# Kernel optimization log

Hardware: AMD Instinct MI355X
Metric: run time of the kernel (lower is better)

The kernel has to match this reference:

```python
import jax, jax.numpy as jnp
import numpy as np

D_MODEL = 1024
N_HEADS = 16
D_K = D_MODEL // N_HEADS
D_FF = 4096
EPS = 1e-5


def setup_inputs() -> dict:
    key = jax.random.key(0)
    ks = jax.random.split(key, 16)
    s = 0.02
    d, f = D_MODEL, D_FF
    return {
        'ebd_x': jax.random.normal(ks[0], (2, 2048, d), jnp.float32),
        'Wq': jax.random.normal(ks[1], (d, d), jnp.float32) * s,
        'bq': jnp.zeros((d,), jnp.float32),
        'Wk': jax.random.normal(ks[2], (d, d), jnp.float32) * s,
        'bk': jnp.zeros((d,), jnp.float32),
        'Wv': jax.random.normal(ks[3], (d, d), jnp.float32) * s,
        'bv': jnp.zeros((d,), jnp.float32),
        'Wo': jax.random.normal(ks[4], (d, d), jnp.float32) * s,
        'bo': jnp.zeros((d,), jnp.float32),
        'W1': jax.random.normal(ks[5], (d, f), jnp.float32) * s,
        'b1': jnp.zeros((f,), jnp.float32),
        'W2': jax.random.normal(ks[6], (f, d), jnp.float32) * s,
        'b2': jnp.zeros((d,), jnp.float32),
        'g1': jnp.ones((d,), jnp.float32),
        'beta1': jnp.zeros((d,), jnp.float32),
        'g2': jnp.ones((d,), jnp.float32),
        'beta2': jnp.zeros((d,), jnp.float32),
    }


def _layernorm(x, g, b):
    mu = jnp.mean(x, axis=-1, keepdims=True)
    var = jnp.mean(jnp.square(x - mu), axis=-1, keepdims=True)
    return (x - mu) * jax.lax.rsqrt(var + EPS) * g + b


def reference(ebd_x, Wq, bq, Wk, bk, Wv, bv, Wo, bo, W1, b1, W2, b2, g1, beta1, g2, beta2):
    b, L, d = ebd_x.shape
    h, dk = N_HEADS, D_K
    # QKV projections, split heads: (b, h, L, dk)
    q = (ebd_x @ Wq + bq).reshape(b, L, h, dk).transpose(0, 2, 1, 3)
    k = (ebd_x @ Wk + bk).reshape(b, L, h, dk).transpose(0, 2, 1, 3)
    v = (ebd_x @ Wv + bv).reshape(b, L, h, dk).transpose(0, 2, 1, 3)
    scores = jnp.einsum('bhLd,bhld->bhLl', q, k) / jnp.sqrt(jnp.float32(dk))
    attn = jax.nn.softmax(scores, axis=-1)
    attn_v = jnp.einsum('bhLl,bhld->bhLd', attn, v)
    # faithful to source: reshape (b,h,L,dk) -> (b,L,d) WITHOUT transposing back
    attn_v = attn_v.reshape(b, L, d)
    attn_v = attn_v @ Wo + bo
    # dropout is identity in eval mode
    x1 = _layernorm(attn_v + ebd_x, g1, beta1)
    ff = jax.nn.gelu(x1 @ W1 + b1, approximate=False) @ W2 + b2
    return _layernorm(ff + x1, g2, beta2)
```

## Files before the change

### kernel.cpp

```cpp
#include <hip/hip_runtime.h>
#include <hip/hip_bf16.h>
#include <math.h>

typedef __bf16 bhalf;
typedef __bf16 bhalf8 __attribute__((ext_vector_type(8)));
typedef float  floatx4 __attribute__((ext_vector_type(4)));
typedef float  floatx8 __attribute__((ext_vector_type(8)));
typedef unsigned short ushort_t;
typedef unsigned short ushort8 __attribute__((ext_vector_type(8)));

#define MFMA16(a, b, c) __builtin_amdgcn_mfma_f32_16x16x32_bf16((a), (b), (c), 0, 0, 0)

__device__ __forceinline__ void gload_lds16(const bhalf* g, bhalf* l)
{
    __builtin_amdgcn_global_load_lds((const __attribute__((address_space(1))) void*)g,
                                     (__attribute__((address_space(3))) void*)l, 16, 0, 0);
}

enum { EPI_PLAIN = 0, EPI_RES = 1, EPI_GELU = 2, EPI_QKV = 3 };

__global__ __launch_bounds__(256) void detect_dtype(const ushort_t* __restrict__ x,
                                                    int* __restrict__ flag)
{
    __shared__ int tot;
    if (threadIdx.x == 0) tot = 0;
    __syncthreads();
    int cnt = 0;
#pragma unroll
    for (int it = 0; it < 8; ++it) {
        const ushort8 u = *(const ushort8*)(x + ((size_t)(it * 256 + threadIdx.x)) * 8);
#pragma unroll
        for (int j = 0; j < 8; j += 2) {
            const int e = (u[j] >> 7) & 0xFF;
            if (e >= 0x90) ++cnt;
        }
    }
    atomicAdd(&tot, cnt);
    __syncthreads();
    if (threadIdx.x == 0) flag[0] = (tot > 64) ? 1 : 0;
}

__global__ __launch_bounds__(256) void norm_x(const void* __restrict__ s,
                                              bhalf* __restrict__ d,
                                              const int* __restrict__ flag)
{
    const int i = (blockIdx.x * 256 + threadIdx.x) * 8;
    if (*flag) {
        const floatx8 v = *(const floatx8*)((const float*)s + i);
        bhalf8 o;
#pragma unroll
        for (int j = 0; j < 8; ++j) o[j] = (bhalf)v[j];
        *(bhalf8*)(d + i) = o;
    } else {
        *(ushort8*)((ushort_t*)d + i) = *(const ushort8*)((const ushort_t*)s + i);
    }
}

struct Cvt { const void* s; bhalf* d; int n; };
struct CvtArr { Cvt t[10]; };

__global__ __launch_bounds__(256) void norm_vec(CvtArr a, const int* __restrict__ flag)
{
    const Cvt c = a.t[blockIdx.y];
    const int i = (blockIdx.x * 256 + threadIdx.x) * 8;
    if (i >= c.n) return;
    if (*flag) {
        const floatx8 v = *(const floatx8*)((const float*)c.s + i);
        bhalf8 o;
#pragma unroll
        for (int j = 0; j < 8; ++j) o[j] = (bhalf)v[j];
        *(bhalf8*)(c.d + i) = o;
    } else {
        *(ushort8*)((ushort_t*)c.d + i) = *(const ushort8*)((const ushort_t*)c.s + i);
    }
}

struct TDesc { const void* src; bhalf* dst; int R, C; };
struct TDescArr { TDesc t[6]; };

__global__ __launch_bounds__(256) void transpose_all(TDescArr a, const int* __restrict__ flag)
{
    __shared__ bhalf sm[32][33];
    const int id = blockIdx.x;
    TDesc d;
    int rem;
    if (id < 4096)      { d = a.t[id >> 10]; rem = id & 1023; }
    else if (id < 8192) { d = a.t[4];        rem = id - 4096; }
    else                { d = a.t[5];        rem = id - 8192; }
    const int txc = d.C >> 5;
    const int bx = (rem % txc) * 32;
    const int by = (rem / txc) * 32;
    const int tx = threadIdx.x & 31;
    const int ty = threadIdx.x >> 5;
    if (*flag) {
        const float* fin = (const float*)d.src;
#pragma unroll
        for (int i = 0; i < 4; ++i)
            sm[ty + i * 8][tx] = (bhalf)fin[(size_t)(by + ty + i * 8) * d.C + bx + tx];
    } else {
        const bhalf* bin = (const bhalf*)d.src;
#pragma unroll
        for (int i = 0; i < 4; ++i)
            sm[ty + i * 8][tx] = bin[(size_t)(by + ty + i * 8) * d.C + bx + tx];
    }
    __syncthreads();
#pragma unroll
    for (int i = 0; i < 4; ++i)
        d.dst[(size_t)(bx + ty + i * 8) * d.R + by + tx] = sm[tx][ty + i * 8];
}

__global__ __launch_bounds__(256) void vt_transpose(const bhalf* __restrict__ Vw,
                                                    bhalf* __restrict__ Vt)
{
    __shared__ bhalf sm[32][33];
    const int bh = blockIdx.z;
    const int b = bh >> 4, h = bh & 15;
    const int tb = blockIdx.y * 32;
    const int db = blockIdx.x * 32;
    const int tx = threadIdx.x & 31;
    const int ty = threadIdx.x >> 5;
#pragma unroll
    for (int i = 0; i < 4; ++i)
        sm[ty + i * 8][tx] = Vw[(size_t)(b * 2048 + tb + ty + i * 8) * 1024 + h * 64 + db + tx];
    __syncthreads();
#pragma unroll
    for (int i = 0; i < 4; ++i)
        Vt[(size_t)(bh * 64 + db + ty + i * 8) * 2048 + tb + tx] = sm[tx][ty + i * 8];
}

template <int EPI, int TN>
__global__ __launch_bounds__(256) void gemm128(
    const bhalf* __restrict__ A, int lda,
    const bhalf* __restrict__ BT, int ldb,
    const bhalf* __restrict__ bias,
    const bhalf* __restrict__ resid,
    bhalf* __restrict__ C, int ldc, int K, int nbx,
    bhalf* __restrict__ Ck, bhalf* __restrict__ Cv)
{
    constexpr int MT = (TN == 128) ? 4 : 2;
    __shared__ __align__(16) bhalf As[2][128 * 64];
    __shared__ __align__(16) bhalf Bs[2][TN * 64];

    const int tid  = threadIdx.x;
    const int lane = tid & 63;
    const int w    = tid >> 6;
    const int l15  = lane & 15;
    const int q    = lane >> 4;
    const int wm   = (TN == 128) ? (w >> 1) * 64 : w * 32;
    const int wn   = (TN == 128) ? (w & 1) * 64 : 0;

    const int nwg = gridDim.x;
    const int cpx = nwg >> 3;
    const int id  = (blockIdx.x & 7) * cpx + (blockIdx.x >> 3);
    const int n0  = (id % nbx) * TN;
    const int m0  = (id / nbx) * 128;

    const int r8 = lane >> 3;
    const int c8 = lane & 7;
    const int gc = (c8 ^ r8) << 3;

    floatx4 acc[MT][4];
#pragma unroll
    for (int i = 0; i < MT; ++i)
#pragma unroll
        for (int j = 0; j < 4; ++j) acc[i][j] = (floatx4){0.f, 0.f, 0.f, 0.f};

    const bhalf* Ab = A  + (size_t)(m0 + r8) * lda + gc;
    const bhalf* Bb = BT + (size_t)(n0 + r8) * ldb + gc;

    auto stage = [&](int buf, int k0) {
#pragma unroll
        for (int i = 0; i < 4; ++i) {
            const int rb = w * 32 + i * 8;
            gload_lds16(Ab + (size_t)rb * lda + k0, &As[buf][rb * 64] + lane * 8);
        }
        if constexpr (TN == 128) {
#pragma unroll
            for (int i = 0; i < 4; ++i) {
                const int rb = w * 32 + i * 8;
                gload_lds16(Bb + (size_t)rb * ldb + k0, &Bs[buf][rb * 64] + lane * 8);
            }
        } else {
#pragma unroll
            for (int i = 0; i < 2; ++i) {
                const int rb = w * 16 + i * 8;
                gload_lds16(Bb + (size_t)rb * ldb + k0, &Bs[buf][rb * 64] + lane * 8);
            }
        }
    };

    auto compute = [&](int buf) {
#pragma unroll
        for (int s = 0; s < 2; ++s) {
            const int pc = (((s * 4 + q) ^ (l15 & 7)) << 3);
            bhalf8 af[MT], bf[4];
#pragma unroll
            for (int mt = 0; mt < MT; ++mt)
                af[mt] = *(const bhalf8*)&As[buf][(wm + mt * 16 + l15) * 64 + pc];
#pragma unroll
            for (int nt = 0; nt < 4; ++nt)
                bf[nt] = *(const bhalf8*)&Bs[buf][(wn + nt * 16 + l15) * 64 + pc];
#pragma unroll
            for (int mt = 0; mt < MT; ++mt)
#pragma unroll
                for (int nt = 0; nt < 4; ++nt)
                    acc[mt][nt] = MFMA16(af[mt], bf[nt], acc[mt][nt]);
        }
    };

    stage(0, 0);
    const int NT = K >> 6;
    for (int t = 0; t < NT; ++t) {
        const int cur = t & 1;
        if (t + 1 < NT) {
            stage(cur ^ 1, (t + 1) << 6);
            if constexpr (TN == 128)
                asm volatile("s_waitcnt vmcnt(8)" ::: "memory");
            else
                asm volatile("s_waitcnt vmcnt(6)" ::: "memory");
        } else {
            asm volatile("s_waitcnt vmcnt(0)" ::: "memory");
        }
        __builtin_amdgcn_s_barrier();
        asm volatile("" ::: "memory");
        compute(cur);
        if (t + 1 < NT) {
            asm volatile("" ::: "memory");
            __builtin_amdgcn_s_barrier();
            asm volatile("" ::: "memory");
        }
    }

#pragma unroll
    for (int mt = 0; mt < MT; ++mt)
#pragma unroll
        for (int nt = 0; nt < 4; ++nt) {
            const int col = n0 + wn + nt * 16 + l15;
            const float bv = (float)bias[col];
#pragma unroll
            for (int r = 0; r < 4; ++r) {
                const int row = m0 + wm + mt * 16 + q * 4 + r;
                float v = acc[mt][nt][r] + bv;
                if constexpr (EPI == EPI_RES) {
                    v += (float)resid[(size_t)row * ldc + col];
                    C[(size_t)row * ldc + col] = (bhalf)v;
                } else if constexpr (EPI == EPI_GELU) {
                    v = 0.5f * v * (1.f + erff(v * 0.70710678118654752f));
                    C[(size_t)row * ldc + col] = (bhalf)v;
                } else if constexpr (EPI == EPI_QKV) {
                    if (col < 1024)       C [(size_t)row * 1024 + col]        = (bhalf)v;
                    else if (col < 2048)  Ck[(size_t)row * 1024 + col - 1024] = (bhalf)v;
                    else                  Cv[(size_t)row * 1024 + col - 2048] = (bhalf)v;
                } else {
                    C[(size_t)row * ldc + col] = (bhalf)v;
                }
            }
        }
}

__global__ __launch_bounds__(256) void flash_attn(
    const bhalf* __restrict__ Q, const bhalf* __restrict__ Km,
    const bhalf* __restrict__ Vt, bhalf* __restrict__ ctx)
{
    __shared__ __align__(16) bhalf Ks[2][64 * 64];
    __shared__ __align__(16) bhalf Vs[2][64 * 64];

    const int tid  = threadIdx.x;
    const int lane = tid & 63;
    const int wq   = tid >> 6;
    const int l15  = lane & 15;
    const int q    = lane >> 4;
    const int bh   = blockIdx.x & 31;
    const int l0   = (blockIdx.x >> 5) * 64;
    const int b    = bh >> 4, h = bh & 15;
    const float SC = 0.125f * 1.44269504f;

    const bhalf* qp = Q + ((size_t)(b * 2048 + l0 + wq * 16 + l15)) * 1024 + h * 64 + q * 8;
    const bhalf8 aQ0 = *(const bhalf8*)qp;
    const bhalf8 aQ1 = *(const bhalf8*)(qp + 32);

    float ps = 0.f;
    floatx4 o[4];
#pragma unroll
    for (int ot = 0; ot < 4; ++ot) o[ot] = (floatx4){0.f, 0.f, 0.f, 0.f};

    const int r8 = lane >> 3;
    const int c8 = lane & 7;
    const bhalf* kbase = Km + ((size_t)(b * 2048)) * 1024 + h * 64;
    const bhalf* vbase = Vt + ((size_t)(bh * 64)) * 2048;

    auto stage = [&](int buf, int kt) {
#pragma unroll
        for (int i = 0; i < 2; ++i) {
            const int rb = wq * 16 + i * 8;
            const int fk = (((rb >> 3) << 1) ^ r8) & 7;
            gload_lds16(kbase + (size_t)(kt + rb + r8) * 1024 + ((c8 ^ fk) << 3),
                        &Ks[buf][rb * 64] + lane * 8);
            gload_lds16(vbase + (size_t)(rb + r8) * 2048 + kt + ((c8 ^ r8) << 3),
                        &Vs[buf][rb * 64] + lane * 8);
        }
    };

    stage(0, 0);
    int cur = 0;
    for (int kt = 0; kt < 2048; kt += 64) {
        __syncthreads();
        if (kt + 64 < 2048) stage(cur ^ 1, kt + 64);

        floatx4 s[4];
#pragma unroll
        for (int nt = 0; nt < 4; ++nt) {
            const int row = (nt >> 1) * 32 + (nt & 1) * 4 + ((l15 >> 2) << 3) + (l15 & 3);
            const int f = (((row >> 3) << 1) ^ row) & 7;
            const bhalf8 k0 = *(const bhalf8*)&Ks[cur][row * 64 + ((q ^ f) << 3)];
            const bhalf8 k1 = *(const bhalf8*)&Ks[cur][row * 64 + (((4 + q) ^ f) << 3)];
            floatx4 z = (floatx4){0.f, 0.f, 0.f, 0.f};
            z = MFMA16(k0, aQ0, z);
            s[nt] = MFMA16(k1, aQ1, z);
        }

        bhalf8 pa[2];
#pragma unroll
        for (int nt = 0; nt < 4; ++nt)
#pragma unroll
            for (int r = 0; r < 4; ++r) {
                const float pv = __builtin_amdgcn_exp2f(fmaf(s[nt][r], SC, -8.f));
                ps += pv;
                pa[nt >> 1][(nt & 1) * 4 + r] = (bhalf)pv;
            }

#pragma unroll
        for (int kc = 0; kc < 2; ++kc)
#pragma unroll
            for (int ot = 0; ot < 4; ++ot) {
                const bhalf8 bV = *(const bhalf8*)&Vs[cur][(ot * 16 + l15) * 64 + (((kc * 4 + q) ^ (l15 & 7)) << 3)];
                o[ot] = MFMA16(pa[kc], bV, o[ot]);
            }
        cur ^= 1;
    }

    ps += __shfl_xor(ps, 16);
    ps += __shfl_xor(ps, 32);
    const float invq = 1.f / ps;
    float inv[4];
#pragma unroll
    for (int r = 0; r < 4; ++r)
        inv[r] = __shfl(invq, (lane & 48) | (q * 4 + r));

#pragma unroll
    for (int ot = 0; ot < 4; ++ot)
#pragma unroll
        for (int r = 0; r < 4; ++r) {
            const int l = l0 + wq * 16 + q * 4 + r;
            const int kk = ot * 16 + l15;
            const int R = h * 128 + (l >> 4);
            const int Cc = (l & 15) * 64 + kk;
            ctx[((size_t)(b * 2048 + R)) * 1024 + Cc] = (bhalf)(o[ot][r] * inv[r]);
        }
}

__global__ __launch_bounds__(256) void ln_kernel(
    const bhalf* __restrict__ X, const bhalf* __restrict__ g,
    const bhalf* __restrict__ be, void* __restrict__ out, const int* __restrict__ flag)
{
    __shared__ float red[4][2];
    const int tid = threadIdx.x;
    const int wid = tid >> 6;
    const int rid = tid >> 7;
    const int lt  = tid & 127;
    const int row = blockIdx.x * 2 + rid;
    const int col = lt * 8;
    const bhalf8 xv = *(const bhalf8*)(X + (size_t)row * 1024 + col);
    float v[8], s1 = 0.f, s2 = 0.f;
#pragma unroll
    for (int i = 0; i < 8; ++i) {
        v[i] = (float)xv[i];
        s1 += v[i];
        s2 += v[i] * v[i];
    }
#pragma unroll
    for (int off = 1; off < 64; off <<= 1) {
        s1 += __shfl_xor(s1, off);
        s2 += __shfl_xor(s2, off);
    }
    if ((tid & 63) == 0) { red[wid][0] = s1; red[wid][1] = s2; }
    __syncthreads();
    const float t1 = red[rid * 2][0] + red[rid * 2 + 1][0];
    const float t2 = red[rid * 2][1] + red[rid * 2 + 1][1];
    const float mu = t1 * (1.f / 1024.f);
    const float rs = rsqrtf(t2 * (1.f / 1024.f) - mu * mu + 1e-5f);
    const bool f32 = flag && (*flag != 0);
    if (f32) {
        floatx8 ov;
#pragma unroll
        for (int i = 0; i < 8; ++i)
            ov[i] = ((v[i] - mu) * rs) * (float)g[col + i] + (float)be[col + i];
        *(floatx8*)((float*)out + (size_t)row * 1024 + col) = ov;
    } else {
        bhalf8 ov;
#pragma unroll
        for (int i = 0; i < 8; ++i)
            ov[i] = (bhalf)(((v[i] - mu) * rs) * (float)g[col + i] + (float)be[col + i]);
        *(bhalf8*)((bhalf*)out + (size_t)row * 1024 + col) = ov;
    }
}

extern "C" void kernel_launch(void* const* d_in, const int* in_sizes, int n_in,
                              void* d_out, int out_size, void* d_ws, size_t ws_size,
                              hipStream_t stream)
{
    (void)in_sizes; (void)n_in; (void)out_size; (void)ws_size;

    char* p = (char*)d_ws;
    const size_t MB = 1024 * 1024;
    int*   flag  = (int*)p;
    bhalf* vecs  = (bhalf*)(p + 128 * 1024);
    bhalf* Qw    = (bhalf*)(p + 1 * MB);
    bhalf* Kw    = (bhalf*)(p + 9 * MB);
    bhalf* Vw    = (bhalf*)(p + 17 * MB);
    bhalf* Vt    = (bhalf*)(p + 25 * MB);
    bhalf* x_n   = (bhalf*)(p + 33 * MB);
    bhalf* WqkvT = (bhalf*)(p + 41 * MB);
    bhalf* WoT   = (bhalf*)(p + 47 * MB);
    bhalf* W1T   = (bhalf*)(p + 49 * MB);
    bhalf* W2T   = (bhalf*)(p + 57 * MB);
    bhalf* ctx   = Vw;
    bhalf* ff1   = (bhalf*)(p + 17 * MB);
    bhalf* ln1   = Qw;
    bhalf* x1    = Kw;
    bhalf* ff2   = Qw;

    bhalf* bqkv  = vecs;
    bhalf* bo_n  = vecs + 1 * 4096;
    bhalf* b1_n  = vecs + 2 * 4096;
    bhalf* b2_n  = vecs + 3 * 4096;
    bhalf* g1_n  = vecs + 4 * 4096;
    bhalf* be1_n = vecs + 5 * 4096;
    bhalf* g2_n  = vecs + 6 * 4096;
    bhalf* be2_n = vecs + 7 * 4096;

    const dim3 blk(256);

    detect_dtype<<<1, blk, 0, stream>>>((const ushort_t*)d_in[0], flag);

    norm_x<<<2048, blk, 0, stream>>>(d_in[0], x_n, flag);
    CvtArr arr;
    arr.t[0] = {d_in[2],  bqkv,        1024};
    arr.t[1] = {d_in[4],  bqkv + 1024, 1024};
    arr.t[2] = {d_in[6],  bqkv + 2048, 1024};
    arr.t[3] = {d_in[8],  bo_n,        1024};
    arr.t[4] = {d_in[10], b1_n,        4096};
    arr.t[5] = {d_in[12], b2_n,        1024};
    arr.t[6] = {d_in[13], g1_n,        1024};
    arr.t[7] = {d_in[14], be1_n,       1024};
    arr.t[8] = {d_in[15], g2_n,        1024};
    arr.t[9] = {d_in[16], be2_n,       1024};
    norm_vec<<<dim3(2, 10), blk, 0, stream>>>(arr, flag);

    TDescArr td;
    td.t[0] = {d_in[1],  WqkvT,               1024, 1024};
    td.t[1] = {d_in[3],  WqkvT + 1024 * 1024, 1024, 1024};
    td.t[2] = {d_in[5],  WqkvT + 2048 * 1024, 1024, 1024};
    td.t[3] = {d_in[7],  WoT,                 1024, 1024};
    td.t[4] = {d_in[9],  W1T,                 1024, 4096};
    td.t[5] = {d_in[11], W2T,                 4096, 1024};
    transpose_all<<<12288, blk, 0, stream>>>(td, flag);

    gemm128<EPI_QKV, 128><<<768, blk, 0, stream>>>(
        x_n, 1024, WqkvT, 1024, bqkv, nullptr, Qw, 1024, 1024, 24, Kw, Vw);

    vt_transpose<<<dim3(2, 64, 32), blk, 0, stream>>>(Vw, Vt);

    flash_attn<<<1024, blk, 0, stream>>>(Qw, Kw, Vt, ctx);

    gemm128<EPI_RES, 64><<<512, blk, 0, stream>>>(
        ctx, 1024, WoT, 1024, bo_n, x_n, ln1, 1024, 1024, 16, nullptr, nullptr);
    ln_kernel<<<2048, blk, 0, stream>>>(ln1, g1_n, be1_n, x1, nullptr);

    gemm128<EPI_GELU, 128><<<1024, blk, 0, stream>>>(
        x1, 1024, W1T, 1024, b1_n, nullptr, ff1, 4096, 1024, 32, nullptr, nullptr);
    gemm128<EPI_RES, 64><<<512, blk, 0, stream>>>(
        ff1, 4096, W2T, 4096, b2_n, x1, ff2, 1024, 4096, 16, nullptr, nullptr);
    ln_kernel<<<2048, blk, 0, stream>>>(ff2, g2_n, be2_n, d_out, flag);
}
```

Baseline: 377.5 us.

## Restructure GEMM into 4-stage K=32 pipeline with precomputed swizzled offsets

The double-buffered K=64 GEMM main loop becomes a four-buffer ring with K=32 slices. Loads run three stages ahead, and the vmcnt waits are tuned per tile shape. LDS and global addresses are precomputed once with a new 4-way XOR swizzle, and the MFMA block is wrapped in s_setprio to favour issue. The aim is to hide global-load latency better, at the cost of twice as many barriers per unit of K and smaller MFMA bursts between syncs.

Result: slower. 414.9 us (+9.9%).

```diff
diff --git a/kernel.cpp b/kernel.cpp
--- a/kernel.cpp
+++ b/kernel.cpp
@@ -129,7 +129,7 @@
 }
 
 template <int EPI, int TN>
-__global__ __launch_bounds__(256) void gemm128(
+__global__ __launch_bounds__(256) void gemm_p4(
     const bhalf* __restrict__ A, int lda,
     const bhalf* __restrict__ BT, int ldb,
     const bhalf* __restrict__ bias,
@@ -137,9 +137,12 @@
     bhalf* __restrict__ C, int ldc, int K, int nbx,
     bhalf* __restrict__ Ck, bhalf* __restrict__ Cv)
 {
-    constexpr int MT = (TN == 128) ? 4 : 2;
-    __shared__ __align__(16) bhalf As[2][128 * 64];
-    __shared__ __align__(16) bhalf Bs[2][TN * 64];
+    constexpr int MT     = (TN == 128) ? 4 : 2;
+    constexpr int BLOADS = (TN == 128) ? 2 : 1;
+    constexpr int WS     = (TN == 128) ? 8 : 6;
+    constexpr int WT     = (TN == 128) ? 4 : 3;
+    __shared__ __align__(16) bhalf As[4][128 * 32];
+    __shared__ __align__(16) bhalf Bs[4][TN * 32];
 
     const int tid  = threadIdx.x;
     const int lane = tid & 63;
@@ -155,9 +158,33 @@
     const int n0  = (id % nbx) * TN;
     const int m0  = (id / nbx) * 128;
 
-    const int r8 = lane >> 3;
-    const int c8 = lane & 7;
-    const int gc = (c8 ^ r8) << 3;
+    const int sr = lane >> 2;
+    const int sl = lane & 3;
+
+    const bhalf* ga[2]; int la[2];
+#pragma unroll
+    for (int i = 0; i < 2; ++i) {
+        const int r = i * 64 + w * 16 + sr;
+        const int c = sl ^ (r & 3) ^ ((r >> 2) & 3);
+        ga[i] = A + (size_t)(m0 + r) * lda + c * 8;
+        la[i] = r * 32 + sl * 8;
+    }
+    const bhalf* gb[BLOADS]; int lb[BLOADS];
+#pragma unroll
+    for (int i = 0; i < BLOADS; ++i) {
+        const int r = (TN == 128) ? (i * 64 + w * 16 + sr) : (w * 16 + sr);
+        const int c = sl ^ (r & 3) ^ ((r >> 2) & 3);
+        gb[i] = BT + (size_t)(n0 + r) * ldb + c * 8;
+        lb[i] = r * 32 + sl * 8;
+    }
+
+    int oa[MT], ob[4];
+#pragma unroll
+    for (int mt = 0; mt < MT; ++mt)
+        oa[mt] = (wm + mt * 16 + l15) * 32 + ((q ^ (l15 & 3) ^ ((l15 >> 2) & 3)) * 8);
+#pragma unroll
+    for (int nt = 0; nt < 4; ++nt)
+        ob[nt] = (wn + nt * 16 + l15) * 32 + ((q ^ (l15 & 3) ^ ((l15 >> 2) & 3)) * 8);
 
     floatx4 acc[MT][4];
 #pragma unroll
@@ -165,70 +192,49 @@
 #pragma unroll
         for (int j = 0; j < 4; ++j) acc[i][j] = (floatx4){0.f, 0.f, 0.f, 0.f};
 
-    const bhalf* Ab = A  + (size_t)(m0 + r8) * lda + gc;
-    const bhalf* Bb = BT + (size_t)(n0 + r8) * ldb + gc;
-
-    auto stage = [&](int buf, int k0) {
-#pragma unroll
-        for (int i = 0; i < 4; ++i) {
-            const int rb = w * 32 + i * 8;
-            gload_lds16(Ab + (size_t)rb * lda + k0, &As[buf][rb * 64] + lane * 8);
-        }
-        if constexpr (TN == 128) {
-#pragma unroll
-            for (int i = 0; i < 4; ++i) {
-                const int rb = w * 32 + i * 8;
-                gload_lds16(Bb + (size_t)rb * ldb + k0, &Bs[buf][rb * 64] + lane * 8);
-            }
-        } else {
-#pragma unroll
-            for (int i = 0; i < 2; ++i) {
-                const int rb = w * 16 + i * 8;
-                gload_lds16(Bb + (size_t)rb * ldb + k0, &Bs[buf][rb * 64] + lane * 8);
-            }
-        }
+    auto stage = [&](int buf, int kt) {
+#pragma unroll
+        for (int i = 0; i < 2; ++i)
+            gload_lds16(ga[i] + kt, &As[buf][la[i]]);
+#pragma unroll
+        for (int i = 0; i < BLOADS; ++i)
+            gload_lds16(gb[i] + kt, &Bs[buf][lb[i]]);
     };
 
     auto compute = [&](int buf) {
-#pragma unroll
-        for (int s = 0; s < 2; ++s) {
-            const int pc = (((s * 4 + q) ^ (l15 & 7)) << 3);
-            bhalf8 af[MT], bf[4];
-#pragma unroll
-            for (int mt = 0; mt < MT; ++mt)
-                af[mt] = *(const bhalf8*)&As[buf][(wm + mt * 16 + l15) * 64 + pc];
+        bhalf8 af[MT], bf[4];
+#pragma unroll
+        for (int mt = 0; mt < MT; ++mt) af[mt] = *(const bhalf8*)&As[buf][oa[mt]];
+#pragma unroll
+        for (int nt = 0; nt < 4; ++nt) bf[nt] = *(const bhalf8*)&Bs[buf][ob[nt]];
+        __builtin_amdgcn_s_setprio(1);
+#pragma unroll
+        for (int mt = 0; mt < MT; ++mt)
 #pragma unroll
             for (int nt = 0; nt < 4; ++nt)
-                bf[nt] = *(const bhalf8*)&Bs[buf][(wn + nt * 16 + l15) * 64 + pc];
-#pragma unroll
-            for (int mt = 0; mt < MT; ++mt)
-#pragma unroll
-                for (int nt = 0; nt < 4; ++nt)
-                    acc[mt][nt] = MFMA16(af[mt], bf[nt], acc[mt][nt]);
-        }
+                acc[mt][nt] = MFMA16(af[mt], bf[nt], acc[mt][nt]);
+        __builtin_amdgcn_s_setprio(0);
     };
 
     stage(0, 0);
-    const int NT = K >> 6;
+    stage(1, 32);
+    stage(2, 64);
+    const int NT = K >> 5;
     for (int t = 0; t < NT; ++t) {
-        const int cur = t & 1;
-        if (t + 1 < NT) {
-            stage(cur ^ 1, (t + 1) << 6);
-            if constexpr (TN == 128)
-                asm volatile("s_waitcnt vmcnt(8)" ::: "memory");
-            else
-                asm volatile("s_waitcnt vmcnt(6)" ::: "memory");
-        } else {
+        if (t + 3 < NT) {
+            stage((t + 3) & 3, (t + 3) << 5);
+            asm volatile("s_waitcnt vmcnt(%0)" :: "i"(WS) : "memory");
+        } else if (t + 3 == NT) {
+            asm volatile("s_waitcnt vmcnt(%0)" :: "i"(WT) : "memory");
+        } else if (t + 2 == NT) {
             asm volatile("s_waitcnt vmcnt(0)" ::: "memory");
         }
         __builtin_amdgcn_s_barrier();
         asm volatile("" ::: "memory");
-        compute(cur);
-        if (t + 1 < NT) {
-            asm volatile("" ::: "memory");
-            __builtin_amdgcn_s_barrier();
-            asm volatile("" ::: "memory");
-        }
+        compute(t & 3);
+        asm volatile("" ::: "memory");
+        __builtin_amdgcn_s_barrier();
+        asm volatile("" ::: "memory");
     }
 
 #pragma unroll
@@ -466,20 +472,20 @@
     td.t[5] = {d_in[11], W2T,                 4096, 1024};
     transpose_all<<<12288, blk, 0, stream>>>(td, flag);
 
-    gemm128<EPI_QKV, 128><<<768, blk, 0, stream>>>(
+    gemm_p4<EPI_QKV, 128><<<768, blk, 0, stream>>>(
         x_n, 1024, WqkvT, 1024, bqkv, nullptr, Qw, 1024, 1024, 24, Kw, Vw);
 
     vt_transpose<<<dim3(2, 64, 32), blk, 0, stream>>>(Vw, Vt);
 
     flash_attn<<<1024, blk, 0, stream>>>(Qw, Kw, Vt, ctx);
 
-    gemm128<EPI_RES, 64><<<512, blk, 0, stream>>>(
+    gemm_p4<EPI_RES, 64><<<512, blk, 0, stream>>>(
         ctx, 1024, WoT, 1024, bo_n, x_n, ln1, 1024, 1024, 16, nullptr, nullptr);
     ln_kernel<<<2048, blk, 0, stream>>>(ln1, g1_n, be1_n, x1, nullptr);
 
-    gemm128<EPI_GELU, 128><<<1024, blk, 0, stream>>>(
+    gemm_p4<EPI_GELU, 128><<<1024, blk, 0, stream>>>(
         x1, 1024, W1T, 1024, b1_n, nullptr, ff1, 4096, 1024, 32, nullptr, nullptr);
-    gemm128<EPI_RES, 64><<<512, blk, 0, stream>>>(
+    gemm_p4<EPI_RES, 64><<<512, blk, 0, stream>>>(
         ff1, 4096, W2T, 4096, b2_n, x1, ff2, 1024, 4096, 16, nullptr, nullptr);
     ln_kernel<<<2048, blk, 0, stream>>>(ff2, g2_n, be2_n, d_out, flag);
 }
```

## Add 512-thread triple-buffered 128x128 GEMM for the W2 down-projection

Applied to the files above, without the earlier changes.

Adds a new gemm_pp kernel with 8 waves per 512-thread block, 128x128 output tiles, a three-stage LDS ring buffer fed by direct global-to-LDS loads with a two-tile prefetch distance, and raised wave priority around the MFMA section. It replaces the 128x64-tile gemm128 launch for the K=4096 FF2 projection, halving the block count to 256 and raising per-block reuse. The aim is to hide global-load latency and improve arithmetic intensity on this long-K GEMM. In exchange it needs 96KB of dynamic LDS (set once through a static attribute call) and leaves only one block per CU on 256 CUs, which may reduce latency hiding.

Result: faster. 369.6 us (-2.1%).

```diff
diff --git a/kernel.cpp b/kernel.cpp
--- a/kernel.cpp
+++ b/kernel.cpp
@@ -235,6 +235,133 @@
     for (int mt = 0; mt < MT; ++mt)
 #pragma unroll
         for (int nt = 0; nt < 4; ++nt) {
+            const int col = n0 + wn + nt * 16 + l15;
+            const float bv = (float)bias[col];
+#pragma unroll
+            for (int r = 0; r < 4; ++r) {
+                const int row = m0 + wm + mt * 16 + q * 4 + r;
+                float v = acc[mt][nt][r] + bv;
+                if constexpr (EPI == EPI_RES) {
+                    v += (float)resid[(size_t)row * ldc + col];
+                    C[(size_t)row * ldc + col] = (bhalf)v;
+                } else if constexpr (EPI == EPI_GELU) {
+                    v = 0.5f * v * (1.f + erff(v * 0.70710678118654752f));
+                    C[(size_t)row * ldc + col] = (bhalf)v;
+                } else if constexpr (EPI == EPI_QKV) {
+                    if (col < 1024)       C [(size_t)row * 1024 + col]        = (bhalf)v;
+                    else if (col < 2048)  Ck[(size_t)row * 1024 + col - 1024] = (bhalf)v;
+                    else                  Cv[(size_t)row * 1024 + col - 2048] = (bhalf)v;
+                } else {
+                    C[(size_t)row * ldc + col] = (bhalf)v;
+                }
+            }
+        }
+}
+
+template <int EPI>
+__global__ __launch_bounds__(512, 2) void gemm_pp(
+    const bhalf* __restrict__ A, int lda,
+    const bhalf* __restrict__ BT, int ldb,
+    const bhalf* __restrict__ bias,
+    const bhalf* __restrict__ resid,
+    bhalf* __restrict__ C, int ldc, int K, int nbx,
+    bhalf* __restrict__ Ck, bhalf* __restrict__ Cv)
+{
+    extern __shared__ __align__(16) bhalf sm[];
+
+    const int tid  = threadIdx.x;
+    const int lane = tid & 63;
+    const int w    = tid >> 6;
+    const int l15  = lane & 15;
+    const int q    = lane >> 4;
+    const int wm   = (w >> 2) * 64;
+    const int wn   = (w & 3) * 32;
+
+    const int nwg = gridDim.x;
+    const int cpx = nwg >> 3;
+    const int id  = (blockIdx.x & 7) * cpx + (blockIdx.x >> 3);
+    const int n0  = (id % nbx) * 128;
+    const int m0  = (id / nbx) * 128;
+
+    const int r6  = tid >> 3;
+    const int c8t = tid & 7;
+    const bhalf* gA[2]; const bhalf* gB[2]; int lA[2], lB[2];
+#pragma unroll
+    for (int i = 0; i < 2; ++i) {
+        const int row = i * 64 + r6;
+        const int gc  = (c8t ^ (r6 & 7)) << 3;
+        gA[i] = A  + (size_t)(m0 + row) * lda + gc;
+        gB[i] = BT + (size_t)(n0 + row) * ldb + gc;
+        lA[i] = row * 64 + c8t * 8;
+        lB[i] = row * 64 + c8t * 8;
+    }
+
+    floatx4 acc[4][2];
+#pragma unroll
+    for (int i = 0; i < 4; ++i)
+#pragma unroll
+        for (int j = 0; j < 2; ++j) acc[i][j] = (floatx4){0.f, 0.f, 0.f, 0.f};
+
+    auto stage = [&](int buf, int k0) {
+        bhalf* as = sm + buf * 8192;
+        bhalf* bs = sm + 24576 + buf * 8192;
+        gload_lds16(gA[0] + k0, as + lA[0]);
+        gload_lds16(gA[1] + k0, as + lA[1]);
+        gload_lds16(gB[0] + k0, bs + lB[0]);
+        gload_lds16(gB[1] + k0, bs + lB[1]);
+    };
+
+    stage(0, 0);
+    stage(1, 64);
+    asm volatile("s_waitcnt vmcnt(4)" ::: "memory");
+    __builtin_amdgcn_s_barrier();
+    asm volatile("" ::: "memory");
+
+    const int NT = K >> 6;
+    for (int t = 0; t < NT; ++t) {
+        const int buf = t % 3;
+        const bhalf* as = sm + buf * 8192;
+        const bhalf* bs = sm + 24576 + buf * 8192;
+
+        bhalf8 af[2][4], bf[2][2];
+#pragma unroll
+        for (int ks = 0; ks < 2; ++ks) {
+            const int pc = (((ks * 4 + q) ^ (l15 & 7)) << 3);
+#pragma unroll
+            for (int mt = 0; mt < 4; ++mt)
+                af[ks][mt] = *(const bhalf8*)&as[(wm + mt * 16 + l15) * 64 + pc];
+#pragma unroll
+            for (int nt = 0; nt < 2; ++nt)
+                bf[ks][nt] = *(const bhalf8*)&bs[(wn + nt * 16 + l15) * 64 + pc];
+        }
+
+        if (t + 2 < NT) stage((t + 2) % 3, (t + 2) << 6);
+
+        __builtin_amdgcn_s_setprio(1);
+#pragma unroll
+        for (int ks = 0; ks < 2; ++ks)
+#pragma unroll
+            for (int mt = 0; mt < 4; ++mt)
+#pragma unroll
+                for (int nt = 0; nt < 2; ++nt)
+                    acc[mt][nt] = MFMA16(af[ks][mt], bf[ks][nt], acc[mt][nt]);
+        __builtin_amdgcn_s_setprio(0);
+
+        if (t + 2 < NT) {
+            asm volatile("s_waitcnt vmcnt(4)" ::: "memory");
+        } else if (t + 1 < NT) {
+            asm volatile("s_waitcnt vmcnt(0)" ::: "memory");
+        }
+        if (t + 1 < NT) {
+            __builtin_amdgcn_s_barrier();
+            asm volatile("" ::: "memory");
+        }
+    }
+
+#pragma unroll
+    for (int mt = 0; mt < 4; ++mt)
+#pragma unroll
+        for (int nt = 0; nt < 2; ++nt) {
             const int col = n0 + wn + nt * 16 + l15;
             const float bv = (float)bias[col];
 #pragma unroll
@@ -439,7 +566,15 @@
     bhalf* g2_n  = vecs + 6 * 4096;
     bhalf* be2_n = vecs + 7 * 4096;
 
+    static bool attr_done = false;
+    if (!attr_done) {
+        hipFuncSetAttribute((const void*)gemm_pp<EPI_RES>,
+                            hipFuncAttributeMaxDynamicSharedMemorySize, 98304);
+        attr_done = true;
+    }
+
     const dim3 blk(256);
+    const dim3 blk512(512);
 
     detect_dtype<<<1, blk, 0, stream>>>((const ushort_t*)d_in[0], flag);
 
@@ -479,7 +614,7 @@
 
     gemm128<EPI_GELU, 128><<<1024, blk, 0, stream>>>(
         x1, 1024, W1T, 1024, b1_n, nullptr, ff1, 4096, 1024, 32, nullptr, nullptr);
-    gemm128<EPI_RES, 64><<<512, blk, 0, stream>>>(
-        ff1, 4096, W2T, 4096, b2_n, x1, ff2, 1024, 4096, 16, nullptr, nullptr);
+    gemm_pp<EPI_RES><<<256, blk512, 98304, stream>>>(
+        ff1, 4096, W2T, 4096, b2_n, x1, ff2, 1024, 4096, 8, nullptr, nullptr);
     ln_kernel<<<2048, blk, 0, stream>>>(ff2, g2_n, be2_n, d_out, flag);
 }
```
